# Kernel optimization log

Hardware: AMD Instinct MI355X
Metric: run time of the kernel (lower is better)

The kernel has to match this reference:

```python
import jax, jax.numpy as jnp
import numpy as np

B, T, C = 2, 2048, 1024
H = 16
D = C // H  # 64
SCALE = 1.0 / np.sqrt(D)


def setup_inputs() -> dict:
    key = jax.random.key(0)
    k1, k2, k3 = jax.random.split(key, 3)
    x = jax.random.normal(k1, (B, T, C), dtype=jnp.float32)
    Wqkv = jax.random.normal(k2, (C, 3 * C), dtype=jnp.float32) * 0.02
    bqkv = jnp.zeros((3 * C,), dtype=jnp.float32)
    Wo = jax.random.normal(k3, (C, C), dtype=jnp.float32) * 0.02
    bo = jnp.zeros((C,), dtype=jnp.float32)
    return {"x": x, "Wqkv": Wqkv, "bqkv": bqkv, "Wo": Wo, "bo": bo}


def reference(x, Wqkv, bqkv, Wo, bo):
    Bsz, Tlen, Cdim = x.shape
    qkv = x @ Wqkv + bqkv                       # [B,T,3C]
    qkv = qkv.reshape(Bsz, Tlen, 3, H, D)
    qkv = jnp.transpose(qkv, (2, 0, 3, 1, 4))   # [3,B,H,T,D]
    q, k, v = qkv[0], qkv[1], qkv[2]
    att = jnp.einsum("bhqd,bhkd->bhqk", q, k) * SCALE
    # NOTE: faithful to source: mask keeps positions where k >= q
    i = jnp.arange(Tlen)
    mask = i[None, :] >= i[:, None]             # [T,T], entry [q,k]: k >= q
    att = jnp.where(mask[None, None], att, -jnp.inf)
    att = jax.nn.softmax(att, axis=-1)
    # dropout p=0.0 (inference) -> identity
    y = jnp.einsum("bhqk,bhkd->bhqd", att, v)   # [B,H,T,D]
    y = jnp.transpose(y, (0, 2, 1, 3)).reshape(Bsz, Tlen, Cdim)
    y = y @ Wo + bo
    return y
```

## Files before the change

### kernel.cpp

```cpp
#include <hip/hip_runtime.h>
#include <hip/hip_bf16.h>
#include <cstdint>
#include <cstddef>

typedef __bf16 bf16_t;
typedef __bf16 bf16x8 __attribute__((ext_vector_type(8)));
typedef __bf16 bf16x4 __attribute__((ext_vector_type(4)));
typedef short short4v __attribute__((ext_vector_type(4)));
typedef float f32x4 __attribute__((ext_vector_type(4)));

#define NB 2
#define NT 2048
#define NC 1024
#define NH 16
#define ND 64
#define NM (NB * NT)
#define N3 (3 * NC)
#define ATT_SCALE 0.125f

#define GLOAD_LDS16(gptr, lptr)                                                          \
  __builtin_amdgcn_global_load_lds((const __attribute__((address_space(1))) void*)(gptr), \
                                   (__attribute__((address_space(3))) void*)(lptr), 16, 0, 0)

__global__ __launch_bounds__(256) void cast_f32_bf16_k(const float* __restrict__ in,
                                                       bf16_t* __restrict__ out, int n) {
  int i = (blockIdx.x * 256 + threadIdx.x) * 4;
  if (i + 3 < n) {
    const float4 v = *(const float4*)(in + i);
    bf16x4 o;
    o[0] = (bf16_t)v.x; o[1] = (bf16_t)v.y; o[2] = (bf16_t)v.z; o[3] = (bf16_t)v.w;
    *(bf16x4*)(out + i) = o;
  }
}

__global__ __launch_bounds__(256) void transpose_cast_k(const float* __restrict__ in,
                                                        bf16_t* __restrict__ out,
                                                        int R, int Ccols) {
  __shared__ float tile[32][33];
  int tc = blockIdx.x * 32;
  int tr = blockIdx.y * 32;
  int lx = threadIdx.x & 31;
  int ly = threadIdx.x >> 5;
#pragma unroll
  for (int i = 0; i < 32; i += 8)
    tile[ly + i][lx] = in[(size_t)(tr + ly + i) * Ccols + tc + lx];
  __syncthreads();
#pragma unroll
  for (int i = 0; i < 32; i += 8)
    out[(size_t)(tc + ly + i) * R + tr + lx] = (bf16_t)tile[lx][ly + i];
}

template <int K>
__device__ __forceinline__ void gemm_mainloop(const bf16_t* __restrict__ A,
                                              const bf16_t* __restrict__ Bt,
                                              int m0, int n0, f32x4 acc[4][4],
                                              bf16_t* lds) {
  bf16_t* As = lds;
  bf16_t* Bs = lds + 4096;
  const int tid = threadIdx.x;
  const int lane = tid & 63;
  const int w = tid >> 6;
  const int wm = (w & 1) * 64;
  const int wn = (w >> 1) * 64;
  const int quad = lane >> 4;
  const int l16 = lane & 15;

  for (int k0 = 0; k0 < K; k0 += 32) {
#pragma unroll
    for (int i = 0; i < 2; ++i) {
      const int gb = w * 128 + i * 64;
      const int g = gb + lane;
      GLOAD_LDS16(A + (size_t)(m0 + (g >> 2)) * K + k0 + (g & 3) * 8, As + gb * 8);
      GLOAD_LDS16(Bt + (size_t)(n0 + (g >> 2)) * K + k0 + (g & 3) * 8, Bs + gb * 8);
    }
    __syncthreads();
    bf16x8 af[4], bfr[4];
#pragma unroll
    for (int i = 0; i < 4; ++i)
      af[i] = *(const bf16x8*)(As + (wm + i * 16 + l16) * 32 + quad * 8);
#pragma unroll
    for (int j = 0; j < 4; ++j)
      bfr[j] = *(const bf16x8*)(Bs + (wn + j * 16 + l16) * 32 + quad * 8);
#pragma unroll
    for (int i = 0; i < 4; ++i)
#pragma unroll
      for (int j = 0; j < 4; ++j)
        acc[i][j] = __builtin_amdgcn_mfma_f32_16x16x32_bf16(af[i], bfr[j], acc[i][j], 0, 0, 0);
    __syncthreads();
  }
}

__global__ __launch_bounds__(256) void qkv_gemm_k(const bf16_t* __restrict__ A,
                                                  const bf16_t* __restrict__ Bt,
                                                  const float* __restrict__ bias,
                                                  bf16_t* __restrict__ qb,
                                                  bf16_t* __restrict__ kb,
                                                  bf16_t* __restrict__ vtb) {
  __shared__ __align__(16) bf16_t lds[8192];
  const int m0 = blockIdx.y * 128, n0 = blockIdx.x * 128;
  f32x4 acc[4][4] = {};
  gemm_mainloop<NC>(A, Bt, m0, n0, acc, lds);

  const int lane = threadIdx.x & 63;
  const int w = threadIdx.x >> 6;
  const int wm = (w & 1) * 64, wn = (w >> 1) * 64;
  const int quad = lane >> 4, l16 = lane & 15;
#pragma unroll
  for (int i = 0; i < 4; ++i)
#pragma unroll
    for (int j = 0; j < 4; ++j) {
      const int n = n0 + wn + j * 16 + l16;
      const float bn = bias[n];
      const int which = n >> 10;
      const int rem = n & 1023;
      const int h = rem >> 6, d = rem & 63;
#pragma unroll
      for (int r = 0; r < 4; ++r) {
        const int m = m0 + wm + i * 16 + quad * 4 + r;
        const int b = m >> 11, t = m & 2047;
        float v = acc[i][j][r] + bn;
        if (which == 0) v *= ATT_SCALE;
        const bf16_t val = (bf16_t)v;
        const size_t bh = (size_t)b * NH + h;
        if (which == 0)
          qb[(bh * NT + t) * ND + d] = val;
        else if (which == 1)
          kb[(bh * NT + t) * ND + d] = val;
        else
          vtb[(bh * ND + d) * NT + t] = val;
      }
    }
}


__device__ __forceinline__ void attn_step(const bf16x8 qf[2],
                                          float& m, float& l, f32x4 o[4],
                                          int qv ,
                                          int t0, bool diag,
                                          const bf16_t* kt, const bf16_t* vt,
                                          int quad, int l16) {
  f32x4 sv[4];
#pragma unroll
  for (int kj = 0; kj < 4; ++kj) {
    const int kr = kj * 16 + l16;
    const int sw = kr & 7;
    f32x4 z = {0.f, 0.f, 0.f, 0.f};
    const bf16x8 a0 = *(const bf16x8*)(kt + (kr * 8 + (quad ^ sw)) * 8);
    z = __builtin_amdgcn_mfma_f32_16x16x32_bf16(a0, qf[0], z, 0, 0, 0);
    const bf16x8 a1 = *(const bf16x8*)(kt + (kr * 8 + ((4 + quad) ^ sw)) * 8);
    z = __builtin_amdgcn_mfma_f32_16x16x32_bf16(a1, qf[1], z, 0, 0, 0);
    sv[kj] = z;
  }
  if (diag) {
#pragma unroll
    for (int kj = 0; kj < 4; ++kj)
#pragma unroll
      for (int r = 0; r < 4; ++r)
        if (t0 + kj * 16 + quad * 4 + r < qv) sv[kj][r] = -INFINITY;
  }
  float mx = -INFINITY;
#pragma unroll
  for (int kj = 0; kj < 4; ++kj)
#pragma unroll
    for (int r = 0; r < 4; ++r) mx = fmaxf(mx, sv[kj][r]);
  mx = fmaxf(mx, __shfl_xor(mx, 16));
  mx = fmaxf(mx, __shfl_xor(mx, 32));
  const float mnew = fmaxf(m, mx);
  const float alpha = __expf(m - mnew);
  m = mnew;
  float s = 0.f;
#pragma unroll
  for (int kj = 0; kj < 4; ++kj)
#pragma unroll
    for (int r = 0; r < 4; ++r) {
      const float p = __expf(sv[kj][r] - mnew);
      sv[kj][r] = p;
      s += p;
    }
  s += __shfl_xor(s, 16);
  s += __shfl_xor(s, 32);
  l = l * alpha + s;
  short4v pf[4];
#pragma unroll
  for (int kj = 0; kj < 4; ++kj) {
    bf16x4 pb;
#pragma unroll
    for (int r = 0; r < 4; ++r) pb[r] = (bf16_t)sv[kj][r];
    pf[kj] = __builtin_bit_cast(short4v, pb);
  }
#pragma unroll
  for (int dj = 0; dj < 4; ++dj) {
    o[dj][0] *= alpha; o[dj][1] *= alpha; o[dj][2] *= alpha; o[dj][3] *= alpha;
    const int dr = dj * 16 + l16;
    const int sw = dr & 7;
#pragma unroll
    for (int kj = 0; kj < 4; ++kj) {
      const int kc = kj * 2 + (quad >> 1);
      const bf16x4 a = *(const bf16x4*)(vt + (dr * 8 + (kc ^ sw)) * 8 + (quad & 1) * 4);
      o[dj] = __builtin_amdgcn_mfma_f32_16x16x16bf16_1k(
          __builtin_bit_cast(short4v, a), pf[kj], o[dj], 0, 0, 0);
    }
  }
}

__global__ __launch_bounds__(256) void attn_k(const bf16_t* __restrict__ q,
                                              const bf16_t* __restrict__ k,
                                              const bf16_t* __restrict__ vt,
                                              bf16_t* __restrict__ y ) {
  const int bh = blockIdx.x >> 4;
  const int p0 = blockIdx.x & 15;
  const int pair = ((blockIdx.x >> 8) & 1) ? (15 - p0) : p0;
  const int tA = pair, tB = 31 - pair;
  const int qA0 = tA * 64, qB0 = tB * 64;
  const int b = bh >> 4, h = bh & 15;
  const bf16_t* qp = q + (size_t)bh * NT * ND;
  const bf16_t* kp = k + (size_t)bh * NT * ND;
  const bf16_t* vp = vt + (size_t)bh * ND * NT;

  __shared__ __align__(16) bf16_t kt[64 * 64];
  __shared__ __align__(16) bf16_t vtile[64 * 64];

  const int lane = threadIdx.x & 63;
  const int w = threadIdx.x >> 6;
  const int quad = lane >> 4, l16 = lane & 15;
  const int qa = qA0 + w * 16 + l16;
  const int qb2 = qB0 + w * 16 + l16;

  bf16x8 qfA[2], qfB[2];
#pragma unroll
  for (int hh = 0; hh < 2; ++hh) {
    qfA[hh] = *(const bf16x8*)(qp + (size_t)qa * ND + hh * 32 + quad * 8);
    qfB[hh] = *(const bf16x8*)(qp + (size_t)qb2 * ND + hh * 32 + quad * 8);
  }

  float mA = -INFINITY, lA = 0.f, mB = -INFINITY, lB = 0.f;
  f32x4 oA[4], oB[4];
#pragma unroll
  for (int dj = 0; dj < 4; ++dj) {
    oA[dj] = (f32x4){0.f, 0.f, 0.f, 0.f};
    oB[dj] = (f32x4){0.f, 0.f, 0.f, 0.f};
  }

  for (int t0 = qA0; t0 < NT; t0 += 64) {
#pragma unroll
    for (int i = 0; i < 2; ++i) {
      const int s = w * 128 + i * 64 + lane;
      const int row = s >> 3;
      const int c = (s & 7) ^ (row & 7);
      GLOAD_LDS16(kp + (size_t)(t0 + row) * ND + c * 8, kt + (w * 128 + i * 64) * 8);
      GLOAD_LDS16(vp + (size_t)row * NT + t0 + c * 8, vtile + (w * 128 + i * 64) * 8);
    }
    __syncthreads();

    attn_step(qfA, mA, lA, oA, qa, t0, t0 == qA0, kt, vtile, quad, l16);
    if (t0 >= qB0)
      attn_step(qfB, mB, lB, oB, qb2, t0, t0 == qB0, kt, vtile, quad, l16);

    __syncthreads();
  }

  const float invA = 1.0f / lA, invB = 1.0f / lB;
  const size_t baseA = ((size_t)b * NT + qa) * NC + h * 64;
  const size_t baseB = ((size_t)b * NT + qb2) * NC + h * 64;
#pragma unroll
  for (int dj = 0; dj < 4; ++dj) {
    bf16x4 va, vb;
#pragma unroll
    for (int r = 0; r < 4; ++r) {
      va[r] = (bf16_t)(oA[dj][r] * invA);
      vb[r] = (bf16_t)(oB[dj][r] * invB);
    }
    *(bf16x4*)(y + baseA + dj * 16 + quad * 4) = va;
    *(bf16x4*)(y + baseB + dj * 16 + quad * 4) = vb;
  }
}

__global__ __launch_bounds__(256) void out_gemm_k(const bf16_t* __restrict__ A,
                                                  const bf16_t* __restrict__ Bt,
                                                  const float* __restrict__ bias,
                                                  float* __restrict__ out) {
  __shared__ __align__(16) bf16_t lds[8192];
  const int m0 = blockIdx.y * 128, n0 = blockIdx.x * 128;
  f32x4 acc[4][4] = {};
  gemm_mainloop<NC>(A, Bt, m0, n0, acc, lds);

  const int lane = threadIdx.x & 63;
  const int w = threadIdx.x >> 6;
  const int wm = (w & 1) * 64, wn = (w >> 1) * 64;
  const int quad = lane >> 4, l16 = lane & 15;
#pragma unroll
  for (int i = 0; i < 4; ++i)
#pragma unroll
    for (int j = 0; j < 4; ++j) {
      const int n = n0 + wn + j * 16 + l16;
      const float bn = bias[n];
#pragma unroll
      for (int r = 0; r < 4; ++r) {
        const int m = m0 + wm + i * 16 + quad * 4 + r;
        out[(size_t)m * NC + n] = acc[i][j][r] + bn;
      }
    }
}

extern "C" void kernel_launch(void* const* d_in, const int* in_sizes, int n_in,
                              void* d_out, int out_size, void* d_ws, size_t ws_size,
                              hipStream_t stream) {
  const float* x = (const float*)d_in[0];
  const float* Wqkv = (const float*)d_in[1];
  const float* bqkv = (const float*)d_in[2];
  const float* Wo = (const float*)d_in[3];
  const float* bo = (const float*)d_in[4];
  float* out = (float*)d_out;

  char* p = (char*)d_ws;
  bf16_t* xbf = (bf16_t*)p;   p += (size_t)NM * NC * sizeof(bf16_t);
  bf16_t* wqkvT = (bf16_t*)p; p += (size_t)N3 * NC * sizeof(bf16_t);
  bf16_t* woT = (bf16_t*)p;   p += (size_t)NC * NC * sizeof(bf16_t);
  bf16_t* qb = (bf16_t*)p;    p += (size_t)NB * NH * NT * ND * sizeof(bf16_t);
  bf16_t* kb = (bf16_t*)p;    p += (size_t)NB * NH * NT * ND * sizeof(bf16_t);
  bf16_t* vtb = (bf16_t*)p;   p += (size_t)NB * NH * ND * NT * sizeof(bf16_t);
  bf16_t* yb = (bf16_t*)p;    p += (size_t)NM * NC * sizeof(bf16_t);

  hipLaunchKernelGGL(cast_f32_bf16_k, dim3(NM * NC / 1024), dim3(256), 0, stream,
                     x, xbf, NM * NC);
  hipLaunchKernelGGL(transpose_cast_k, dim3(N3 / 32, NC / 32), dim3(256), 0, stream,
                     Wqkv, wqkvT, NC, N3);
  hipLaunchKernelGGL(transpose_cast_k, dim3(NC / 32, NC / 32), dim3(256), 0, stream,
                     Wo, woT, NC, NC);
  hipLaunchKernelGGL(qkv_gemm_k, dim3(N3 / 128, NM / 128), dim3(256), 0, stream,
                     xbf, wqkvT, bqkv, qb, kb, vtb);
  hipLaunchKernelGGL(attn_k, dim3(32 * 16), dim3(256), 0, stream,
                     qb, kb, vtb, yb);
  hipLaunchKernelGGL(out_gemm_k, dim3(NC / 128, NM / 128), dim3(256), 0, stream,
                     yb, woT, bo, out);
}
```

Baseline: 204.8 us.

## Restructure attention to per-wave independent tiles reading K/V directly from global

The attention kernel now gives each wave its own 16-row query tile, balanced across waves by pairing early and late tiles. Each wave reads K and a pre-tiled V layout straight from global/L2 instead of staging them through LDS with block-wide barriers. A new vtile_k kernel rearranges V into an MFMA-friendly chunked layout, reusing the x-bf16 buffer. Q is prescaled by scale·log2e so the softmax can use exp2f. The change removes syncthreads and LDS staging and raises the grid to 1024 blocks, at the cost of an extra kernel pass and redundant global reads of K/V across waves.

```diff
diff --git a/kernel.cpp b/kernel.cpp
--- a/kernel.cpp
+++ b/kernel.cpp
@@ -16,7 +16,7 @@
 #define ND 64
 #define NM (NB * NT)
 #define N3 (3 * NC)
-#define ATT_SCALE 0.125f
+#define QSCALE_LOG2E 0.18033688011112042f
 
 #define GLOAD_LDS16(gptr, lptr)                                                          \
   __builtin_amdgcn_global_load_lds((const __attribute__((address_space(1))) void*)(gptr), \
@@ -95,7 +95,7 @@
                                                   const float* __restrict__ bias,
                                                   bf16_t* __restrict__ qb,
                                                   bf16_t* __restrict__ kb,
-                                                  bf16_t* __restrict__ vtb) {
+                                                  bf16_t* __restrict__ vb) {
   __shared__ __align__(16) bf16_t lds[8192];
   const int m0 = blockIdx.y * 128, n0 = blockIdx.x * 128;
   f32x4 acc[4][4] = {};
@@ -114,164 +114,134 @@
       const int which = n >> 10;
       const int rem = n & 1023;
       const int h = rem >> 6, d = rem & 63;
+      bf16_t* dst = (which == 0) ? qb : (which == 1) ? kb : vb;
+      const float sc = (which == 0) ? QSCALE_LOG2E : 1.0f;
 #pragma unroll
       for (int r = 0; r < 4; ++r) {
         const int m = m0 + wm + i * 16 + quad * 4 + r;
         const int b = m >> 11, t = m & 2047;
-        float v = acc[i][j][r] + bn;
-        if (which == 0) v *= ATT_SCALE;
-        const bf16_t val = (bf16_t)v;
         const size_t bh = (size_t)b * NH + h;
-        if (which == 0)
-          qb[(bh * NT + t) * ND + d] = val;
-        else if (which == 1)
-          kb[(bh * NT + t) * ND + d] = val;
-        else
-          vtb[(bh * ND + d) * NT + t] = val;
+        dst[(bh * NT + t) * ND + d] = (bf16_t)((acc[i][j][r] + bn) * sc);
       }
     }
 }
 
-
-__device__ __forceinline__ void attn_step(const bf16x8 qf[2],
-                                          float& m, float& l, f32x4 o[4],
-                                          int qv ,
-                                          int t0, bool diag,
-                                          const bf16_t* kt, const bf16_t* vt,
-                                          int quad, int l16) {
-  f32x4 sv[4];
-#pragma unroll
-  for (int kj = 0; kj < 4; ++kj) {
-    const int kr = kj * 16 + l16;
-    const int sw = kr & 7;
-    f32x4 z = {0.f, 0.f, 0.f, 0.f};
-    const bf16x8 a0 = *(const bf16x8*)(kt + (kr * 8 + (quad ^ sw)) * 8);
-    z = __builtin_amdgcn_mfma_f32_16x16x32_bf16(a0, qf[0], z, 0, 0, 0);
-    const bf16x8 a1 = *(const bf16x8*)(kt + (kr * 8 + ((4 + quad) ^ sw)) * 8);
-    z = __builtin_amdgcn_mfma_f32_16x16x32_bf16(a1, qf[1], z, 0, 0, 0);
-    sv[kj] = z;
-  }
-  if (diag) {
-#pragma unroll
-    for (int kj = 0; kj < 4; ++kj)
-#pragma unroll
-      for (int r = 0; r < 4; ++r)
-        if (t0 + kj * 16 + quad * 4 + r < qv) sv[kj][r] = -INFINITY;
-  }
-  float mx = -INFINITY;
-#pragma unroll
-  for (int kj = 0; kj < 4; ++kj)
-#pragma unroll
-    for (int r = 0; r < 4; ++r) mx = fmaxf(mx, sv[kj][r]);
-  mx = fmaxf(mx, __shfl_xor(mx, 16));
-  mx = fmaxf(mx, __shfl_xor(mx, 32));
-  const float mnew = fmaxf(m, mx);
-  const float alpha = __expf(m - mnew);
-  m = mnew;
-  float s = 0.f;
-#pragma unroll
-  for (int kj = 0; kj < 4; ++kj)
-#pragma unroll
-    for (int r = 0; r < 4; ++r) {
-      const float p = __expf(sv[kj][r] - mnew);
-      sv[kj][r] = p;
-      s += p;
-    }
-  s += __shfl_xor(s, 16);
-  s += __shfl_xor(s, 32);
-  l = l * alpha + s;
-  short4v pf[4];
-#pragma unroll
-  for (int kj = 0; kj < 4; ++kj) {
-    bf16x4 pb;
-#pragma unroll
-    for (int r = 0; r < 4; ++r) pb[r] = (bf16_t)sv[kj][r];
-    pf[kj] = __builtin_bit_cast(short4v, pb);
-  }
-#pragma unroll
-  for (int dj = 0; dj < 4; ++dj) {
-    o[dj][0] *= alpha; o[dj][1] *= alpha; o[dj][2] *= alpha; o[dj][3] *= alpha;
-    const int dr = dj * 16 + l16;
-    const int sw = dr & 7;
-#pragma unroll
-    for (int kj = 0; kj < 4; ++kj) {
-      const int kc = kj * 2 + (quad >> 1);
-      const bf16x4 a = *(const bf16x4*)(vt + (dr * 8 + (kc ^ sw)) * 8 + (quad & 1) * 4);
-      o[dj] = __builtin_amdgcn_mfma_f32_16x16x16bf16_1k(
-          __builtin_bit_cast(short4v, a), pf[kj], o[dj], 0, 0, 0);
-    }
-  }
-}
-
-__global__ __launch_bounds__(256) void attn_k(const bf16_t* __restrict__ q,
-                                              const bf16_t* __restrict__ k,
-                                              const bf16_t* __restrict__ vt,
-                                              bf16_t* __restrict__ y ) {
-  const int bh = blockIdx.x >> 4;
-  const int p0 = blockIdx.x & 15;
-  const int pair = ((blockIdx.x >> 8) & 1) ? (15 - p0) : p0;
-  const int tA = pair, tB = 31 - pair;
-  const int qA0 = tA * 64, qB0 = tB * 64;
+__global__ __launch_bounds__(256) void vtile_k(const bf16_t* __restrict__ v,
+                                               bf16_t* __restrict__ vt2) {
+  const int bh = blockIdx.x >> 5, c = blockIdx.x & 31;
+  const bf16_t* src = v + ((size_t)bh * NT + c * 64) * ND;
+  bf16_t* dst = vt2 + ((size_t)bh * 32 + c) * 4096;
+#pragma unroll
+  for (int it = 0; it < 4; ++it) {
+    const int slot = it * 256 + threadIdx.x;
+    const int g = slot >> 6, d = slot & 63;
+    bf16x4 val;
+#pragma unroll
+    for (int j = 0; j < 4; ++j) val[j] = src[(size_t)(g * 4 + j) * ND + d];
+    *(bf16x4*)(dst + (size_t)slot * 4) = val;
+  }
+}
+
+__global__ __launch_bounds__(256, 4) void attn_k(const bf16_t* __restrict__ q,
+                                                 const bf16_t* __restrict__ k,
+                                                 const bf16_t* __restrict__ vt2,
+                                                 bf16_t* __restrict__ y ) {
+  const int bh = blockIdx.x & 31;
+  const int s = blockIdx.x >> 5;
+  const int w = threadIdx.x >> 6;
+  const int tile = (w >> 1) * 64 + ((w & 1) ? (63 - s) : s);
+  const int lane = threadIdx.x & 63;
+  const int quad = lane >> 4, l16 = lane & 15;
+  const int qv = tile * 16 + l16;
   const int b = bh >> 4, h = bh & 15;
+
   const bf16_t* qp = q + (size_t)bh * NT * ND;
   const bf16_t* kp = k + (size_t)bh * NT * ND;
-  const bf16_t* vp = vt + (size_t)bh * ND * NT;
-
-  __shared__ __align__(16) bf16_t kt[64 * 64];
-  __shared__ __align__(16) bf16_t vtile[64 * 64];
-
-  const int lane = threadIdx.x & 63;
-  const int w = threadIdx.x >> 6;
-  const int quad = lane >> 4, l16 = lane & 15;
-  const int qa = qA0 + w * 16 + l16;
-  const int qb2 = qB0 + w * 16 + l16;
-
-  bf16x8 qfA[2], qfB[2];
-#pragma unroll
-  for (int hh = 0; hh < 2; ++hh) {
-    qfA[hh] = *(const bf16x8*)(qp + (size_t)qa * ND + hh * 32 + quad * 8);
-    qfB[hh] = *(const bf16x8*)(qp + (size_t)qb2 * ND + hh * 32 + quad * 8);
-  }
-
-  float mA = -INFINITY, lA = 0.f, mB = -INFINITY, lB = 0.f;
-  f32x4 oA[4], oB[4];
+  const bf16_t* vp = vt2 + (size_t)bh * 32 * 4096;
+
+  const bf16x8 qf0 = *(const bf16x8*)(qp + (size_t)qv * ND + quad * 8);
+  const bf16x8 qf1 = *(const bf16x8*)(qp + (size_t)qv * ND + 32 + quad * 8);
+
+  float m = -INFINITY, l = 0.f;
+  f32x4 o[4];
+#pragma unroll
+  for (int dj = 0; dj < 4; ++dj) o[dj] = (f32x4){0.f, 0.f, 0.f, 0.f};
+
+  const int c0 = tile >> 2;
+  for (int c = c0; c < 32; ++c) {
+    const int t0 = c * 64;
+    const bf16_t* kc = kp + (size_t)t0 * ND;
+    const bf16_t* vc = vp + (size_t)c * 4096;
+
+    f32x4 sv[4];
+#pragma unroll
+    for (int kj = 0; kj < 4; ++kj) {
+      const bf16_t* krow = kc + (size_t)(kj * 16 + l16) * ND;
+      const bf16x8 a0 = *(const bf16x8*)(krow + quad * 8);
+      const bf16x8 a1 = *(const bf16x8*)(krow + 32 + quad * 8);
+      f32x4 z = {0.f, 0.f, 0.f, 0.f};
+      z = __builtin_amdgcn_mfma_f32_16x16x32_bf16(a0, qf0, z, 0, 0, 0);
+      z = __builtin_amdgcn_mfma_f32_16x16x32_bf16(a1, qf1, z, 0, 0, 0);
+      sv[kj] = z;
+    }
+    if (c == c0) {
+#pragma unroll
+      for (int kj = 0; kj < 4; ++kj)
+#pragma unroll
+        for (int r = 0; r < 4; ++r)
+          if (t0 + kj * 16 + quad * 4 + r < qv) sv[kj][r] = -INFINITY;
+    }
+    float mx = -INFINITY;
+#pragma unroll
+    for (int kj = 0; kj < 4; ++kj)
+#pragma unroll
+      for (int r = 0; r < 4; ++r) mx = fmaxf(mx, sv[kj][r]);
+    mx = fmaxf(mx, __shfl_xor(mx, 16));
+    mx = fmaxf(mx, __shfl_xor(mx, 32));
+    const float mnew = fmaxf(m, mx);
+    const float alpha = exp2f(m - mnew);
+    m = mnew;
+    float rs = 0.f;
+#pragma unroll
+    for (int kj = 0; kj < 4; ++kj)
+#pragma unroll
+      for (int r = 0; r < 4; ++r) {
+        const float p = exp2f(sv[kj][r] - mnew);
+        sv[kj][r] = p;
+        rs += p;
+      }
+    rs += __shfl_xor(rs, 16);
+    rs += __shfl_xor(rs, 32);
+    l = l * alpha + rs;
+    short4v pf[4];
+#pragma unroll
+    for (int kj = 0; kj < 4; ++kj) {
+      bf16x4 pb;
+#pragma unroll
+      for (int r = 0; r < 4; ++r) pb[r] = (bf16_t)sv[kj][r];
+      pf[kj] = __builtin_bit_cast(short4v, pb);
+    }
+#pragma unroll
+    for (int dj = 0; dj < 4; ++dj) {
+      o[dj][0] *= alpha; o[dj][1] *= alpha; o[dj][2] *= alpha; o[dj][3] *= alpha;
+#pragma unroll
+      for (int kj = 0; kj < 4; ++kj) {
+        const bf16x4 a =
+            *(const bf16x4*)(vc + ((size_t)(kj * 4 + quad) * 64 + dj * 16 + l16) * 4);
+        o[dj] = __builtin_amdgcn_mfma_f32_16x16x16bf16_1k(
+            __builtin_bit_cast(short4v, a), pf[kj], o[dj], 0, 0, 0);
+      }
+    }
+  }
+
+  const float inv = 1.0f / l;
+  const size_t base = ((size_t)b * NT + qv) * NC + h * 64;
 #pragma unroll
   for (int dj = 0; dj < 4; ++dj) {
-    oA[dj] = (f32x4){0.f, 0.f, 0.f, 0.f};
-    oB[dj] = (f32x4){0.f, 0.f, 0.f, 0.f};
-  }
-
-  for (int t0 = qA0; t0 < NT; t0 += 64) {
-#pragma unroll
-    for (int i = 0; i < 2; ++i) {
-      const int s = w * 128 + i * 64 + lane;
-      const int row = s >> 3;
-      const int c = (s & 7) ^ (row & 7);
-      GLOAD_LDS16(kp + (size_t)(t0 + row) * ND + c * 8, kt + (w * 128 + i * 64) * 8);
-      GLOAD_LDS16(vp + (size_t)row * NT + t0 + c * 8, vtile + (w * 128 + i * 64) * 8);
-    }
-    __syncthreads();
-
-    attn_step(qfA, mA, lA, oA, qa, t0, t0 == qA0, kt, vtile, quad, l16);
-    if (t0 >= qB0)
-      attn_step(qfB, mB, lB, oB, qb2, t0, t0 == qB0, kt, vtile, quad, l16);
-
-    __syncthreads();
-  }
-
-  const float invA = 1.0f / lA, invB = 1.0f / lB;
-  const size_t baseA = ((size_t)b * NT + qa) * NC + h * 64;
-  const size_t baseB = ((size_t)b * NT + qb2) * NC + h * 64;
-#pragma unroll
-  for (int dj = 0; dj < 4; ++dj) {
-    bf16x4 va, vb;
-#pragma unroll
-    for (int r = 0; r < 4; ++r) {
-      va[r] = (bf16_t)(oA[dj][r] * invA);
-      vb[r] = (bf16_t)(oB[dj][r] * invB);
-    }
-    *(bf16x4*)(y + baseA + dj * 16 + quad * 4) = va;
-    *(bf16x4*)(y + baseB + dj * 16 + quad * 4) = vb;
+    bf16x4 va;
+#pragma unroll
+    for (int r = 0; r < 4; ++r) va[r] = (bf16_t)(o[dj][r] * inv);
+    *(bf16x4*)(y + base + dj * 16 + quad * 4) = va;
   }
 }
 
@@ -318,8 +288,9 @@
   bf16_t* woT = (bf16_t*)p;   p += (size_t)NC * NC * sizeof(bf16_t);
   bf16_t* qb = (bf16_t*)p;    p += (size_t)NB * NH * NT * ND * sizeof(bf16_t);
   bf16_t* kb = (bf16_t*)p;    p += (size_t)NB * NH * NT * ND * sizeof(bf16_t);
-  bf16_t* vtb = (bf16_t*)p;   p += (size_t)NB * NH * ND * NT * sizeof(bf16_t);
+  bf16_t* vb = (bf16_t*)p;    p += (size_t)NB * NH * NT * ND * sizeof(bf16_t);
   bf16_t* yb = (bf16_t*)p;    p += (size_t)NM * NC * sizeof(bf16_t);
+  bf16_t* vt2 = xbf;
 
   hipLaunchKernelGGL(cast_f32_bf16_k, dim3(NM * NC / 1024), dim3(256), 0, stream,
                      x, xbf, NM * NC);
@@ -328,9 +299,9 @@
   hipLaunchKernelGGL(transpose_cast_k, dim3(NC / 32, NC / 32), dim3(256), 0, stream,
                      Wo, woT, NC, NC);
   hipLaunchKernelGGL(qkv_gemm_k, dim3(N3 / 128, NM / 128), dim3(256), 0, stream,
-                     xbf, wqkvT, bqkv, qb, kb, vtb);
-  hipLaunchKernelGGL(attn_k, dim3(32 * 16), dim3(256), 0, stream,
-                     qb, kb, vtb, yb);
+                     xbf, wqkvT, bqkv, qb, kb, vb);
+  hipLaunchKernelGGL(vtile_k, dim3(32 * 32), dim3(256), 0, stream, vb, vt2);
+  hipLaunchKernelGGL(attn_k, dim3(1024), dim3(256), 0, stream, qb, kb, vt2, yb);
   hipLaunchKernelGGL(out_gemm_k, dim3(NC / 128, NM / 128), dim3(256), 0, stream,
                      yb, woT, bo, out);
 }
```

After: 245.4 us. 19.8% more time.
